# Optimization experiments

Hardware: AMD Instinct MI355X
Metric: run time of the kernel (lower is better)

## Reference

```python
import jax, jax.numpy as jnp
import numpy as np

N, EMB, ATT = 65536, 1024, 512


def setup_inputs() -> dict:
    key = jax.random.key(0)
    k = jax.random.split(key, 6)
    scale = 0.02
    return {
        "leaves": jax.random.normal(k[0], (N, EMB), dtype=jnp.float32),
        "ancestors": jax.random.normal(k[1], (N, EMB), dtype=jnp.float32),
        "W1": jax.random.normal(k[2], (2 * EMB, ATT), dtype=jnp.float32) * scale,
        "b1": jax.random.normal(k[3], (ATT,), dtype=jnp.float32) * scale,
        "W2": jax.random.normal(k[4], (ATT, 1), dtype=jnp.float32) * scale,
        "b2": jax.random.normal(k[5], (1,), dtype=jnp.float32) * scale,
    }


def reference(leaves, ancestors, W1, b1, W2, b2):
    # concat -> [N, 2*EMB]
    x = jnp.concatenate([leaves, ancestors], axis=-1)
    # additive attention MLP: linear -> tanh -> linear -> [N, 1]
    h = jnp.tanh(x @ W1 + b1)
    scores = h @ W2 + b2            # [N, 1]
    attn = jax.nn.softmax(scores, axis=0)  # softmax over the pair dim
    # reshape to [1, N], matmul ancestors [N, EMB] -> [1, EMB], sum dim 0 -> [EMB]
    out = jnp.squeeze(attn, axis=1) @ ancestors  # [EMB]
    return out
```

## Files before the change

kernel.cpp:

```cpp
#include <hip/hip_runtime.h>
#include <hip/hip_bf16.h>
#include <stdint.h>
#include <stddef.h>

typedef __bf16 bf16;
typedef bf16 bf16x8 __attribute__((ext_vector_type(8)));
typedef float f32x4 __attribute__((ext_vector_type(4)));

#define N_ROWS 65536
#define EMB    1024
#define ATTD   512
#define KDIM   2048
#define BM     128
#define BN     128
#define BK     64
#define NKB    (KDIM / BK)
#define MBLK   (N_ROWS / BM)
#define NSPL   (ATTD / BN)

__device__ __forceinline__ void gload_lds16(const void* g, void* l) {
  __builtin_amdgcn_global_load_lds(
      (const __attribute__((address_space(1))) void*)g,
      (__attribute__((address_space(3))) void*)l, 16, 0, 0);
}

__global__ __launch_bounds__(256) void k_prep_w1(const float* __restrict__ W1,
                                                 bf16* __restrict__ W1t) {
  __shared__ float tile[64][132];
  const int kb = blockIdx.x;
  const int bn = blockIdx.y;
  const int t  = threadIdx.x;

  const int kr = t >> 2;
  const int nc = (t & 3) * 32;
  const float* src = W1 + (size_t)(kb * 64 + kr) * ATTD + bn * 128 + nc;
  #pragma unroll
  for (int q = 0; q < 8; ++q) {
    float4 v = *(const float4*)(src + q * 4);
    tile[kr][nc + q * 4 + 0] = v.x;
    tile[kr][nc + q * 4 + 1] = v.y;
    tile[kr][nc + q * 4 + 2] = v.z;
    tile[kr][nc + q * 4 + 3] = v.w;
  }
  __syncthreads();

  const int n  = t >> 1;
  const int pb = (t & 1) * 4;
  bf16* dst = W1t + (size_t)(kb * 4 + bn) * (BN * BK);
  #pragma unroll
  for (int pi = 0; pi < 4; ++pi) {
    const int c    = pb + pi;
    const int frag = (((n >> 6) * 4) + ((n >> 4) & 3)) * 2 + (c >> 2);
    const int lane = (c & 3) * 16 + (n & 15);
    bf16x8 o;
    #pragma unroll
    for (int e = 0; e < 8; ++e) o[e] = (bf16)tile[c * 8 + e][n];
    *(bf16x8*)(dst + frag * 512 + lane * 8) = o;
  }
}

__global__ __launch_bounds__(256, 3) void k_gemm_score(
    const float* __restrict__ leaves, const float* __restrict__ anc,
    const bf16* __restrict__ W1t, const float* __restrict__ b1,
    const float* __restrict__ W2, float* __restrict__ spart) {
  __shared__ float ldsAf[BM * BK];

  const int t    = threadIdx.x;
  const int lane = t & 63;
  const int wave = t >> 6;
  const int l15  = lane & 15;
  const int l4   = lane >> 4;
  const int wm2  = wave >> 1;
  const int wn2  = wave & 1;

  const int g   = blockIdx.x;
  const int sb  = g >> 5;
  const int q   = g & 31;
  const int bn  = q >> 3;
  const int bm  = sb * 8 + (q & 7);
  const int m0  = bm * BM;
  const int n0  = bn * BN;

  const int a_rbase = t >> 4;
  const int a_koff  = ((t & 15) ^ ((t >> 4) & 7)) * 4;

  int a_rd_lo[2][4], a_rd_hi[2][4];
  #pragma unroll
  for (int ks = 0; ks < 2; ++ks) {
    #pragma unroll
    for (int mi = 0; mi < 4; ++mi) {
      const int row = wm2 * 64 + mi * 16 + l15;
      const int c   = ks * 4 + l4;
      const int s3  = row & 7;
      a_rd_lo[ks][mi] = row * BK + ((2 * c)     ^ s3) * 4;
      a_rd_hi[ks][mi] = row * BK + ((2 * c + 1) ^ s3) * 4;
    }
  }

  const f32x4 zero4 = {0.f, 0.f, 0.f, 0.f};
  f32x4 acc[4][4];
  #pragma unroll
  for (int i = 0; i < 4; ++i)
    #pragma unroll
    for (int j = 0; j < 4; ++j) acc[i][j] = zero4;

  const bf16* Bbase = W1t + (size_t)bn * (BN * BK) + (wn2 * 8) * 512 + lane * 8;

  for (int kb = 0; kb < NKB; ++kb) {
    const float* Abase = (kb < 16)
        ? leaves + (size_t)m0 * EMB + (size_t)kb * BK
        : anc    + (size_t)m0 * EMB + (size_t)(kb - 16) * BK;
    #pragma unroll
    for (int s = 0; s < 8; ++s) {
      const int r = s * 16 + a_rbase;
      gload_lds16(Abase + (size_t)r * EMB + a_koff,
                  ldsAf + (s * 256 + t) * 4);
    }
    bf16x8 B[8];
    {
      const bf16* bp = Bbase + (size_t)kb * (4 * BN * BK);
      #pragma unroll
      for (int f = 0; f < 8; ++f)
        B[f] = *(const bf16x8*)(bp + f * 512);
    }
    __syncthreads();
    #pragma unroll
    for (int ks = 0; ks < 2; ++ks) {
      bf16x8 af[4];
      #pragma unroll
      for (int mi = 0; mi < 4; ++mi) {
        f32x4 lo = *(const f32x4*)(ldsAf + a_rd_lo[ks][mi]);
        f32x4 hi = *(const f32x4*)(ldsAf + a_rd_hi[ks][mi]);
        af[mi] = (bf16x8){(bf16)lo.x, (bf16)lo.y, (bf16)lo.z, (bf16)lo.w,
                          (bf16)hi.x, (bf16)hi.y, (bf16)hi.z, (bf16)hi.w};
      }
      #pragma unroll
      for (int ni = 0; ni < 4; ++ni)
        #pragma unroll
        for (int mi = 0; mi < 4; ++mi)
          acc[mi][ni] = __builtin_amdgcn_mfma_f32_16x16x32_bf16(
              af[mi], B[ni * 2 + ks], acc[mi][ni], 0, 0, 0);
    }
    __syncthreads();
  }

  float b1c[4], w2c[4];
  #pragma unroll
  for (int ni = 0; ni < 4; ++ni) {
    const int col = n0 + wn2 * 64 + ni * 16 + l15;
    b1c[ni] = b1[col];
    w2c[ni] = W2[col];
  }
  float* sp = ldsAf;
  #pragma unroll
  for (int mi = 0; mi < 4; ++mi) {
    #pragma unroll
    for (int r = 0; r < 4; ++r) {
      float p = 0.f;
      #pragma unroll
      for (int ni = 0; ni < 4; ++ni)
        p += tanhf(acc[mi][ni][r] + b1c[ni]) * w2c[ni];
      p += __shfl_xor(p, 1);
      p += __shfl_xor(p, 2);
      p += __shfl_xor(p, 4);
      p += __shfl_xor(p, 8);
      if (l15 == 0) sp[wn2 * 128 + wm2 * 64 + mi * 16 + l4 * 4 + r] = p;
    }
  }
  __syncthreads();
  if (t < BM)
    spart[(size_t)bn * N_ROWS + m0 + t] = sp[t] + sp[128 + t];
}

__global__ __launch_bounds__(128) void k_combine(
    const float* __restrict__ spart, const float* __restrict__ b2,
    float* __restrict__ scores, float* __restrict__ bmax,
    float* __restrict__ bsum) {
  const int b = blockIdx.x, t = threadIdx.x;
  const int lane = t & 63, wave = t >> 6;
  const int m = b * 128 + t;
  __shared__ float rm[2], rs[2];
  const float s = spart[m] + spart[N_ROWS + m] + spart[2 * N_ROWS + m] +
                  spart[3 * N_ROWS + m] + b2[0];
  scores[m] = s;
  float mm = s;
  #pragma unroll
  for (int o = 32; o; o >>= 1) mm = fmaxf(mm, __shfl_xor(mm, o));
  if (lane == 0) rm[wave] = mm;
  __syncthreads();
  const float bM = fmaxf(rm[0], rm[1]);
  float ee = __expf(s - bM);
  #pragma unroll
  for (int o = 32; o; o >>= 1) ee += __shfl_xor(ee, o);
  if (lane == 0) rs[wave] = ee;
  __syncthreads();
  if (t == 0) {
    bmax[b] = bM;
    bsum[b] = rs[0] + rs[1];
  }
}

__global__ __launch_bounds__(512) void k_mz(const float* __restrict__ bmax,
                                            const float* __restrict__ bsum,
                                            float* __restrict__ MZ,
                                            float* __restrict__ scale) {
  const int t = threadIdx.x, lane = t & 63, wave = t >> 6;
  __shared__ float rm[8], rs[8];
  const float m = bmax[t];
  float mm = m;
  #pragma unroll
  for (int o = 32; o; o >>= 1) mm = fmaxf(mm, __shfl_xor(mm, o));
  if (lane == 0) rm[wave] = mm;
  __syncthreads();
  if (t == 0) {
    float g = rm[0];
    for (int i = 1; i < 8; ++i) g = fmaxf(g, rm[i]);
    rm[0] = g;
  }
  __syncthreads();
  const float M = rm[0];
  const float sc = __expf(m - M);
  scale[t] = sc;
  float z = bsum[t] * sc;
  #pragma unroll
  for (int o = 32; o; o >>= 1) z += __shfl_xor(z, o);
  if (lane == 0) rs[wave] = z;
  __syncthreads();
  if (t == 0) {
    float Z = 0.f;
    for (int i = 0; i < 8; ++i) Z += rs[i];
    MZ[0] = M;
    MZ[1] = Z;
  }
}

__global__ __launch_bounds__(256) void k_part(const float* __restrict__ anc,
                                              const float* __restrict__ scores,
                                              const float* __restrict__ bmax,
                                              float* __restrict__ part) {
  __shared__ float w[BM];
  const int b = blockIdx.x, t = threadIdx.x;
  const float bM = bmax[b];
  if (t < BM) w[t] = __expf(scores[(size_t)b * BM + t] - bM);
  __syncthreads();
  float4 a = {0.f, 0.f, 0.f, 0.f};
  const float4* src = (const float4*)(anc + (size_t)b * BM * EMB) + t;
  #pragma unroll 4
  for (int i = 0; i < BM; ++i) {
    float4 v = src[i * (EMB / 4)];
    const float wi = w[i];
    a.x += wi * v.x;
    a.y += wi * v.y;
    a.z += wi * v.z;
    a.w += wi * v.w;
  }
  ((float4*)(part + (size_t)b * EMB))[t] = a;
}

__global__ __launch_bounds__(256) void k_final(const float* __restrict__ part,
                                               const float* __restrict__ scale,
                                               const float* __restrict__ MZ,
                                               float* __restrict__ out) {
  const int j = blockIdx.x * 256 + threadIdx.x;
  float s0 = 0.f, s1 = 0.f, s2 = 0.f, s3 = 0.f;
  for (int b = 0; b < MBLK; b += 4) {
    s0 += part[(size_t)(b + 0) * EMB + j] * scale[b + 0];
    s1 += part[(size_t)(b + 1) * EMB + j] * scale[b + 1];
    s2 += part[(size_t)(b + 2) * EMB + j] * scale[b + 2];
    s3 += part[(size_t)(b + 3) * EMB + j] * scale[b + 3];
  }
  out[j] = (s0 + s1 + s2 + s3) / MZ[1];
}

extern "C" void kernel_launch(void* const* d_in, const int* in_sizes, int n_in,
                              void* d_out, int out_size, void* d_ws,
                              size_t ws_size, hipStream_t stream) {
  const float* leaves = (const float*)d_in[0];
  const float* anc    = (const float*)d_in[1];
  const float* W1     = (const float*)d_in[2];
  const float* b1     = (const float*)d_in[3];
  const float* W2     = (const float*)d_in[4];
  const float* b2     = (const float*)d_in[5];
  float* out = (float*)d_out;

  char* ws = (char*)d_ws;
  bf16*  W1t    = (bf16*)ws;
  float* spart  = (float*)(ws + (2u << 20));
  float* scores = (float*)(ws + (3u << 20));
  float* bmax   = (float*)(ws + (3u << 20) + (1u << 18));
  float* bsum   = bmax + MBLK;
  float* scale  = bsum + MBLK;
  float* MZ     = scale + MBLK;
  float* part   = (float*)(ws + (4u << 20));

  k_prep_w1<<<dim3(32, 4), 256, 0, stream>>>(W1, W1t);
  k_gemm_score<<<dim3(MBLK * NSPL), 256, 0, stream>>>(leaves, anc, W1t, b1, W2,
                                                      spart);
  k_combine<<<dim3(MBLK), 128, 0, stream>>>(spart, b2, scores, bmax, bsum);
  k_mz<<<dim3(1), 512, 0, stream>>>(bmax, bsum, MZ, scale);
  k_part<<<dim3(MBLK), 256, 0, stream>>>(anc, scores, bmax, part);
  k_final<<<dim3(EMB / 256), 256, 0, stream>>>(part, scale, MZ, out);
}
```

Measured before the change: 306.6 us.

## Double-buffer A tile in LDS to overlap global loads with MFMA

Splits the fp32 A staging buffer in LDS into two halves. The async global-to-LDS loads for the next K block are issued before the current block's MFMA work, and a prologue load fills the first buffer. This is meant to hide global load latency behind compute and drops one barrier per iteration. In exchange, LDS per block doubles and the launch bound falls from 3 to 2 blocks per CU, which reduces occupancy.

```diff
diff --git a/kernel.cpp b/kernel.cpp
--- a/kernel.cpp
+++ b/kernel.cpp
@@ -59,11 +59,11 @@
   }
 }
 
-__global__ __launch_bounds__(256, 3) void k_gemm_score(
+__global__ __launch_bounds__(256, 2) void k_gemm_score(
     const float* __restrict__ leaves, const float* __restrict__ anc,
     const bf16* __restrict__ W1t, const float* __restrict__ b1,
     const float* __restrict__ W2, float* __restrict__ spart) {
-  __shared__ float ldsAf[BM * BK];
+  __shared__ float ldsAf[2][BM * BK];
 
   const int t    = threadIdx.x;
   const int lane = t & 63;
@@ -106,16 +106,25 @@
 
   const bf16* Bbase = W1t + (size_t)bn * (BN * BK) + (wn2 * 8) * 512 + lane * 8;
 
+#define ISSUE_A(KB, BUF)                                                       \
+  do {                                                                         \
+    const float* Abase_ = ((KB) < 16)                                          \
+        ? leaves + (size_t)m0 * EMB + (size_t)(KB)*BK                          \
+        : anc    + (size_t)m0 * EMB + (size_t)((KB) - 16) * BK;                \
+    _Pragma("unroll")                                                          \
+    for (int s_ = 0; s_ < 8; ++s_) {                                           \
+      const int r_ = s_ * 16 + a_rbase;                                        \
+      gload_lds16(Abase_ + (size_t)r_ * EMB + a_koff,                          \
+                  &ldsAf[BUF][(s_ * 256 + t) * 4]);                            \
+    }                                                                          \
+  } while (0)
+
+  ISSUE_A(0, 0);
+  __syncthreads();
+
   for (int kb = 0; kb < NKB; ++kb) {
-    const float* Abase = (kb < 16)
-        ? leaves + (size_t)m0 * EMB + (size_t)kb * BK
-        : anc    + (size_t)m0 * EMB + (size_t)(kb - 16) * BK;
-    #pragma unroll
-    for (int s = 0; s < 8; ++s) {
-      const int r = s * 16 + a_rbase;
-      gload_lds16(Abase + (size_t)r * EMB + a_koff,
-                  ldsAf + (s * 256 + t) * 4);
-    }
+    const int cur = kb & 1;
+    if (kb + 1 < NKB) ISSUE_A(kb + 1, cur ^ 1);
     bf16x8 B[8];
     {
       const bf16* bp = Bbase + (size_t)kb * (4 * BN * BK);
@@ -123,14 +132,13 @@
       for (int f = 0; f < 8; ++f)
         B[f] = *(const bf16x8*)(bp + f * 512);
     }
-    __syncthreads();
     #pragma unroll
     for (int ks = 0; ks < 2; ++ks) {
       bf16x8 af[4];
       #pragma unroll
       for (int mi = 0; mi < 4; ++mi) {
-        f32x4 lo = *(const f32x4*)(ldsAf + a_rd_lo[ks][mi]);
-        f32x4 hi = *(const f32x4*)(ldsAf + a_rd_hi[ks][mi]);
+        f32x4 lo = *(const f32x4*)(&ldsAf[cur][a_rd_lo[ks][mi]]);
+        f32x4 hi = *(const f32x4*)(&ldsAf[cur][a_rd_hi[ks][mi]]);
         af[mi] = (bf16x8){(bf16)lo.x, (bf16)lo.y, (bf16)lo.z, (bf16)lo.w,
                           (bf16)hi.x, (bf16)hi.y, (bf16)hi.z, (bf16)hi.w};
       }
@@ -143,6 +151,7 @@
     }
     __syncthreads();
   }
+#undef ISSUE_A
 
   float b1c[4], w2c[4];
   #pragma unroll
@@ -151,7 +160,7 @@
     b1c[ni] = b1[col];
     w2c[ni] = W2[col];
   }
-  float* sp = ldsAf;
+  float* sp = &ldsAf[0][0];
   #pragma unroll
   for (int mi = 0; mi < 4; ++mi) {
     #pragma unroll
```

Measured after the change: 406.6 us. 1.33x slower.
